# Kernel optimization log

Measured on AMD Instinct MI355X. Metric: run time of the kernel, lower is better.

The kernel has to match this reference:

```python
import jax, jax.numpy as jnp
import numpy as np

B, N, E = 256, 50000, 128000


def setup_inputs() -> dict:
    key = jax.random.key(0)
    ks = jax.random.split(key, 12)
    # forward args (normalized predictions / demand truth)
    pred_p_norm = jax.random.normal(ks[0], (B, N), dtype=jnp.float32)
    pred_f_norm = jax.random.normal(ks[1], (B, E), dtype=jnp.float32)
    true_d_norm = jax.random.normal(ks[2], (B, N), dtype=jnp.float32)
    # scaler params (positive scales)
    p_mean = jax.random.normal(ks[3], (N,), dtype=jnp.float32) * 10.0 + 50.0
    p_scale = jax.random.uniform(ks[4], (N,), dtype=jnp.float32, minval=0.5, maxval=5.0)
    f_mean = jax.random.normal(ks[5], (E,), dtype=jnp.float32) * 0.1
    f_scale = jax.random.uniform(ks[6], (E,), dtype=jnp.float32, minval=0.01, maxval=1.0)
    d_mean = jax.random.normal(ks[7], (N,), dtype=jnp.float32) * 0.01
    d_scale = jax.random.uniform(ks[8], (N,), dtype=jnp.float32, minval=0.001, maxval=0.1)
    node_elevation = jax.random.uniform(ks[9], (N,), dtype=jnp.float32, minval=0.0, maxval=300.0)
    # edge static attrs -> Hazen-Williams resistance R = 10.67 * L * (C+eps)^-1.852 * (D+eps)^-4.87
    L = jax.random.uniform(ks[10], (E,), dtype=jnp.float32, minval=10.0, maxval=1000.0)
    D = jax.random.uniform(ks[11], (E,), dtype=jnp.float32, minval=0.05, maxval=1.0)
    C = jnp.full((E,), 130.0, dtype=jnp.float32)
    eps = 1e-06
    R = 10.67 * L * (C + eps) ** (-1.852) * (D + eps) ** (-4.87)
    edge_index = jax.random.randint(jax.random.fold_in(key, 99), (2, E), 0, N, dtype=jnp.int32)
    return {
        'pred_p_norm': pred_p_norm, 'pred_f_norm': pred_f_norm, 'true_d_norm': true_d_norm,
        'p_mean': p_mean, 'p_scale': p_scale, 'f_mean': f_mean, 'f_scale': f_scale,
        'd_mean': d_mean, 'd_scale': d_scale, 'node_elevation': node_elevation,
        'R': R, 'edge_index': edge_index,
    }


def reference(pred_p_norm, pred_f_norm, true_d_norm, p_mean, p_scale, f_mean, f_scale,
              d_mean, d_scale, node_elevation, R, edge_index):
    n_nodes = pred_p_norm.shape[1]
    # denormalize (broadcast per-node / per-edge scalers over batch)
    P = pred_p_norm * p_scale[None, :] + p_mean[None, :]          # [B, N]
    Q = pred_f_norm * f_scale[None, :] + f_mean[None, :]          # [B, E]
    d = true_d_norm * d_scale[None, :] + d_mean[None, :]          # [B, N]
    H = P + node_elevation[None, :]                               # hydraulic head [B, N]
    src, dst = edge_index[0], edge_index[1]
    # mass conservation: net inflow per node vs demand
    Q_T = Q.T                                                      # [E, B]
    q_out = jax.ops.segment_sum(Q_T, src, num_segments=n_nodes).T  # [B, N]
    q_in = jax.ops.segment_sum(Q_T, dst, num_segments=n_nodes).T   # [B, N]
    q_net = q_in - q_out
    loss_mass = jnp.mean((q_net - d) ** 2)
    # head loss (Hazen-Williams): delta_h vs R*Q*|Q|^0.852
    h_src = H[:, src]                                              # [B, E]
    h_dst = H[:, dst]                                              # [B, E]
    delta_h_pred = h_src - h_dst
    friction_slope = R[None, :] * Q * jnp.abs(Q) ** 0.852
    loss_head = jnp.mean((delta_h_pred - friction_slope) ** 2)
    return (loss_mass, loss_head)
```

## Files before the change

kernel.cpp:

```cpp
#include <hip/hip_runtime.h>
#include <hip/hip_fp16.h>

#define TILE 64

__global__ void k_build_ht(const float* __restrict__ pred_p,
                           const float* __restrict__ p_scale,
                           const float* __restrict__ p_mean,
                           const float* __restrict__ elev,
                           const float* __restrict__ true_d,
                           const float* __restrict__ d_scale,
                           const float* __restrict__ d_mean,
                           __half* __restrict__ HTh,
                           __half* __restrict__ TD,
                           int B, int N) {
    __shared__ __align__(16) float tile[TILE][TILE + 2];
    const int n0 = blockIdx.x * TILE;
    const int b0 = blockIdx.y * TILE;
    const int tn = threadIdx.x % TILE;
    const int tw = threadIdx.x / TILE;
    const int c  = threadIdx.x & 31;
    const int rg = threadIdx.x >> 5;
    const int n = n0 + tn;

    {
        float sc = 0.f, mn = 0.f, el = 0.f;
        if (n < N) { sc = p_scale[n]; mn = p_mean[n]; el = elev[n]; }
        #pragma unroll
        for (int i = 0; i < TILE / 4; ++i) {
            const int bl = i * 4 + tw;
            float v = 0.f;
            if (n < N) v = pred_p[(size_t)(b0 + bl) * N + n] * sc + mn + el;
            tile[tn][bl] = v;
        }
        __syncthreads();
        #pragma unroll
        for (int i = 0; i < 8; ++i) {
            const int nl = i * 8 + rg;
            const int nn = n0 + nl;
            if (nn < N) {
                const float2 f = *reinterpret_cast<const float2*>(&tile[nl][2 * c]);
                reinterpret_cast<__half2*>(HTh + (size_t)nn * B + b0)[c] =
                    __floats2half2_rn(f.x, f.y);
            }
        }
    }
    __syncthreads();
    {
        float sc = 0.f, mn = 0.f;
        if (n < N) { sc = d_scale[n]; mn = d_mean[n]; }
        #pragma unroll
        for (int i = 0; i < TILE / 4; ++i) {
            const int bl = i * 4 + tw;
            float v = 0.f;
            if (n < N) v = true_d[(size_t)(b0 + bl) * N + n] * sc + mn;
            tile[tn][bl] = v;
        }
        __syncthreads();
        #pragma unroll
        for (int i = 0; i < 8; ++i) {
            const int nl = i * 8 + rg;
            const int nn = n0 + nl;
            if (nn < N) {
                const float2 f = *reinterpret_cast<const float2*>(&tile[nl][2 * c]);
                reinterpret_cast<__half2*>(TD + (size_t)nn * B + b0)[c] =
                    __floats2half2_rn(f.x, f.y);
            }
        }
    }
}

__global__ void k_hist(const int* __restrict__ nodes, int* __restrict__ deg, int M) {
    const int i = blockIdx.x * 256 + threadIdx.x;
    if (i < M) atomicAdd(&deg[nodes[i]], 1);
}

__global__ void k_scan1(const int* __restrict__ deg, int* __restrict__ bsum, int N) {
    __shared__ int s[256];
    const int i = blockIdx.x * 256 + threadIdx.x;
    s[threadIdx.x] = (i < N) ? deg[i] : 0;
    __syncthreads();
    #pragma unroll
    for (int off = 128; off >= 1; off >>= 1) {
        if (threadIdx.x < off) s[threadIdx.x] += s[threadIdx.x + off];
        __syncthreads();
    }
    if (threadIdx.x == 0) bsum[blockIdx.x] = s[0];
}

__global__ void k_scan2(int* __restrict__ bsum, int nb) {
    __shared__ int s[256];
    const int t = threadIdx.x;
    const int v = (t < nb) ? bsum[t] : 0;
    s[t] = v;
    __syncthreads();
    #pragma unroll
    for (int off = 1; off < 256; off <<= 1) {
        const int tmp = (t >= off) ? s[t - off] : 0;
        __syncthreads();
        s[t] += tmp;
        __syncthreads();
    }
    if (t < nb) bsum[t] = s[t] - v;
}

__global__ void k_scan3(const int* __restrict__ deg, const int* __restrict__ bsum,
                        int* __restrict__ offsets, int* __restrict__ cursor, int N) {
    __shared__ int s[256];
    const int t = threadIdx.x;
    const int i = blockIdx.x * 256 + t;
    const int v = (i < N) ? deg[i] : 0;
    s[t] = v;
    __syncthreads();
    #pragma unroll
    for (int off = 1; off < 256; off <<= 1) {
        const int tmp = (t >= off) ? s[t - off] : 0;
        __syncthreads();
        s[t] += tmp;
        __syncthreads();
    }
    const int excl = s[t] - v + bsum[blockIdx.x];
    if (i < N) { offsets[i] = excl; cursor[i] = excl; }
    if (i == N - 1) offsets[N] = excl + v;
}

__global__ void k_fill(const int* __restrict__ esrc, const int* __restrict__ edst,
                       int* __restrict__ cursor, int* __restrict__ inc, int E) {
    const int e = blockIdx.x * 256 + threadIdx.x;
    if (e < E) {
        const int ps = atomicAdd(&cursor[esrc[e]], 1);
        inc[ps] = (e << 1);
        const int pd = atomicAdd(&cursor[edst[e]], 1);
        inc[pd] = (e << 1) | 1;
    }
}

__global__ void k_edges(const float* __restrict__ pred_f,
                        const float* __restrict__ f_scale,
                        const float* __restrict__ f_mean,
                        const float* __restrict__ Rcoef,
                        const int* __restrict__ esrc,
                        const int* __restrict__ edst,
                        const __half* __restrict__ HTh,
                        __half* __restrict__ QT,
                        double* __restrict__ headp,
                        int B, int E) {
    __shared__ __align__(16) float qt[TILE][TILE + 2];
    __shared__ double wsum[4];
    const int e0 = blockIdx.x * TILE;
    const int b0 = blockIdx.y * TILE;
    const int te = threadIdx.x % TILE;
    const int tw = threadIdx.x / TILE;

    const int e = e0 + te;
    const float fs = f_scale[e];
    const float fm = f_mean[e];
    #pragma unroll
    for (int i = 0; i < TILE / 4; ++i) {
        const int bl = i * 4 + tw;
        qt[te][bl] = pred_f[(size_t)(b0 + bl) * E + e] * fs + fm;
    }
    __syncthreads();

    const int bl = te;
    const __half* HTb = HTh + b0 + bl;

    int   sarr[16], darr[16];
    float hs[16], hd[16];
    #pragma unroll
    for (int j = 0; j < 16; ++j) {
        const int ee = e0 + tw * 16 + j;
        sarr[j] = esrc[ee];
        darr[j] = edst[ee];
        hs[j] = __half2float(HTb[(size_t)sarr[j] * B]);
        hd[j] = __half2float(HTb[(size_t)darr[j] * B]);
    }

    const int sel = bl >> 5;
    const int pc  = bl & 31;
    #pragma unroll
    for (int k = 0; k < 8; ++k) {
        const int el = tw * 16 + 2 * k + sel;
        const float2 q01 = *reinterpret_cast<const float2*>(&qt[el][2 * pc]);
        const __half2 h = __floats2half2_rn(q01.x, q01.y);
        *reinterpret_cast<__half2*>(
            (char*)QT + (size_t)(e0 + el) * B * 2 + (size_t)b0 * 2 + pc * 4) = h;
    }

    double head = 0.0;
    #pragma unroll
    for (int j = 0; j < 16; ++j) {
        const int el = tw * 16 + j;
        const int ee = e0 + el;
        const float q = qt[el][bl];
        const float aq = fabsf(q);
        const float pw = exp2f(0.852f * __log2f(aq));
        const float fr = Rcoef[ee] * q * pw;
        const float t = (hs[j] - hd[j]) - fr;
        head += (double)t * (double)t;
    }

    #pragma unroll
    for (int off = 32; off >= 1; off >>= 1)
        head += __shfl_down(head, off, 64);
    if ((threadIdx.x & 63) == 0) wsum[threadIdx.x >> 6] = head;
    __syncthreads();
    if (threadIdx.x == 0)
        headp[(size_t)blockIdx.y * gridDim.x + blockIdx.x] =
            wsum[0] + wsum[1] + wsum[2] + wsum[3];
}

__global__ __launch_bounds__(256) void k_nodemass(
        const __half* __restrict__ QT,
        const __half* __restrict__ TD,
        const int* __restrict__ offsets,
        const int* __restrict__ inc,
        double* __restrict__ massp,
        int N) {
    __shared__ double wsum[4];
    const int w = threadIdx.x >> 6;
    const int lane = threadIdx.x & 63;
    const int n = blockIdx.x * 4 + w;

    double m = 0.0;
    if (n < N) {
        const uint2 tdr = *reinterpret_cast<const uint2*>(
            (const char*)TD + (size_t)n * 512 + (size_t)lane * 8);

        const int beg = offsets[n];
        const int end = offsets[n + 1];

        float qn0 = 0.f, qn1 = 0.f, qn2 = 0.f, qn3 = 0.f;
        for (int k = beg; k < end; k += 8) {
            int   ivv[8];
            float sg[8];
            uint2 vv[8];
            #pragma unroll
            for (int u = 0; u < 8; ++u) {
                const int kk = (k + u < end) ? (k + u) : (end - 1);
                ivv[u] = inc[kk];
                sg[u] = (k + u < end) ? ((ivv[u] & 1) ? 1.f : -1.f) : 0.f;
                vv[u] = *reinterpret_cast<const uint2*>(
                    (const char*)QT + (size_t)(ivv[u] >> 1) * 512
                                    + (size_t)lane * 8);
            }
            #pragma unroll
            for (int u = 0; u < 8; ++u) {
                const __half2 a = *reinterpret_cast<const __half2*>(&vv[u].x);
                const __half2 b = *reinterpret_cast<const __half2*>(&vv[u].y);
                const float2 fa = __half22float2(a);
                const float2 fb = __half22float2(b);
                qn0 += sg[u] * fa.x; qn1 += sg[u] * fa.y;
                qn2 += sg[u] * fb.x; qn3 += sg[u] * fb.y;
            }
        }

        const __half2 d01 = *reinterpret_cast<const __half2*>(&tdr.x);
        const __half2 d23 = *reinterpret_cast<const __half2*>(&tdr.y);
        const float2 f01 = __half22float2(d01);
        const float2 f23 = __half22float2(d23);
        const float t0 = qn0 - f01.x;
        const float t1 = qn1 - f01.y;
        const float t2 = qn2 - f23.x;
        const float t3 = qn3 - f23.y;
        m = (double)t0 * t0 + (double)t1 * t1
          + (double)t2 * t2 + (double)t3 * t3;
    }

    #pragma unroll
    for (int off = 32; off >= 1; off >>= 1)
        m += __shfl_down(m, off, 64);
    if (lane == 0) wsum[w] = m;
    __syncthreads();
    if (threadIdx.x == 0)
        massp[blockIdx.x] = wsum[0] + wsum[1] + wsum[2] + wsum[3];
}

__global__ void k_reduce(const double* __restrict__ massp, int nm,
                         const double* __restrict__ headp, int nh,
                         float* __restrict__ out,
                         double inv_mass, double inv_head) {
    __shared__ double sh[256];
    const int t = threadIdx.x;

    double s = 0.0;
    for (int i = t; i < nm; i += 256) s += massp[i];
    sh[t] = s;
    __syncthreads();
    #pragma unroll
    for (int off = 128; off >= 1; off >>= 1) {
        if (t < off) sh[t] += sh[t + off];
        __syncthreads();
    }
    double mass_total = 0.0;
    if (t == 0) mass_total = sh[0];
    __syncthreads();

    s = 0.0;
    for (int i = t; i < nh; i += 256) s += headp[i];
    sh[t] = s;
    __syncthreads();
    #pragma unroll
    for (int off = 128; off >= 1; off >>= 1) {
        if (t < off) sh[t] += sh[t + off];
        __syncthreads();
    }
    if (t == 0) {
        out[0] = (float)(mass_total * inv_mass);
        out[1] = (float)(sh[0] * inv_head);
    }
}

static inline size_t align256s(size_t x) { return (x + 255) & ~(size_t)255; }

extern "C" void kernel_launch(void* const* d_in, const int* in_sizes, int n_in,
                              void* d_out, int out_size, void* d_ws, size_t ws_size,
                              hipStream_t stream) {
    const float* pred_p  = (const float*)d_in[0];
    const float* pred_f  = (const float*)d_in[1];
    const float* true_d  = (const float*)d_in[2];
    const float* p_mean  = (const float*)d_in[3];
    const float* p_scale = (const float*)d_in[4];
    const float* f_mean  = (const float*)d_in[5];
    const float* f_scale = (const float*)d_in[6];
    const float* d_mean  = (const float*)d_in[7];
    const float* d_scale = (const float*)d_in[8];
    const float* elev    = (const float*)d_in[9];
    const float* Rcoef   = (const float*)d_in[10];
    const int*   eidx    = (const int*)d_in[11];

    const int N = in_sizes[3];
    const int E = in_sizes[10];
    const int B = in_sizes[0] / N;

    const int* esrc = eidx;
    const int* edst = eidx + E;

    const int gn = (N + TILE - 1) / TILE;
    const int gb = B / TILE;
    const int ge = E / TILE;
    const int nbk = (N + 255) / 256;
    const int nmB = (N + 3) / 4;

    char* ws = (char*)d_ws;
    size_t off = 0;
    __half* HTh   = (__half*)(ws + off); off = align256s(off + (size_t)N * B * 2);
    __half* TD    = (__half*)(ws + off); off = align256s(off + (size_t)N * B * 2);
    __half* QT    = (__half*)(ws + off); off = align256s(off + (size_t)E * B * 2);
    int* incarr   = (int*)(ws + off);    off = align256s(off + (size_t)2 * E * 4);
    int* offsets  = (int*)(ws + off);    off = align256s(off + (size_t)(N + 1) * 4);
    int* cursor   = (int*)(ws + off);    off = align256s(off + (size_t)N * 4);
    double* headp = (double*)(ws + off); off = align256s(off + (size_t)ge * gb * 8);
    double* massp = (double*)(ws + off); off = align256s(off + (size_t)nmB * 8);
    const size_t zero_beg = off;
    int* deg      = (int*)(ws + off);    off = align256s(off + (size_t)N * 4);
    int* bsum     = (int*)(ws + off);    off = align256s(off + 256 * 4);
    const size_t zero_len = off - zero_beg;

    hipMemsetAsync(ws + zero_beg, 0, zero_len, stream);

    k_hist <<<(2 * E + 255) / 256, 256, 0, stream>>>(eidx, deg, 2 * E);
    k_scan1<<<nbk, 256, 0, stream>>>(deg, bsum, N);
    k_scan2<<<1, 256, 0, stream>>>(bsum, nbk);
    k_scan3<<<nbk, 256, 0, stream>>>(deg, bsum, offsets, cursor, N);
    k_fill <<<(E + 255) / 256, 256, 0, stream>>>(esrc, edst, cursor, incarr, E);

    k_build_ht<<<dim3(gn, gb), 256, 0, stream>>>(pred_p, p_scale, p_mean, elev,
                                                 true_d, d_scale, d_mean,
                                                 HTh, TD, B, N);
    k_edges<<<dim3(ge, gb), 256, 0, stream>>>(pred_f, f_scale, f_mean, Rcoef,
                                              esrc, edst, HTh, QT,
                                              headp, B, E);
    k_nodemass<<<nmB, 256, 0, stream>>>(QT, TD, offsets, incarr, massp, N);
    k_reduce<<<1, 256, 0, stream>>>(massp, nmB, headp, ge * gb,
                                    (float*)d_out,
                                    1.0 / ((double)B * (double)N),
                                    1.0 / ((double)B * (double)E));
}
```

Measured before the change: 181.0 us.

## Restructure edge kernel over full batch, fuse histogram into build kernel

The edge kernel now processes all 256 batch columns per block. It stages Q as half in shared memory and gathers 8-byte rows of H per lane, so each src/dst index is read once instead of being re-gathered for each of four batch tiles with scalar half loads. The degree histogram is folded into the H/TD build kernel to remove one launch, and the node-mass kernel gets a short path for nodes with four or fewer incident edges. The cost is larger shared memory per block (about 50 KB) and fewer blocks in the edge kernel, which may lower occupancy.

```diff
diff --git a/kernel.cpp b/kernel.cpp
--- a/kernel.cpp
+++ b/kernel.cpp
@@ -10,6 +10,9 @@
                            const float* __restrict__ true_d,
                            const float* __restrict__ d_scale,
                            const float* __restrict__ d_mean,
+                           const int* __restrict__ nodes,
+                           int* __restrict__ deg,
+                           int M,
                            __half* __restrict__ HTh,
                            __half* __restrict__ TD,
                            int B, int N) {
@@ -22,6 +25,12 @@
     const int rg = threadIdx.x >> 5;
     const int n = n0 + tn;
 
+    const int flat = blockIdx.y * gridDim.x + blockIdx.x;
+    if (flat < (M + 255) / 256) {
+        const int i = flat * 256 + threadIdx.x;
+        if (i < M) atomicAdd(&deg[nodes[i]], 1);
+    }
+
     {
         float sc = 0.f, mn = 0.f, el = 0.f;
         if (n < N) { sc = p_scale[n]; mn = p_mean[n]; el = elev[n]; }
@@ -69,11 +78,6 @@
     }
 }
 
-__global__ void k_hist(const int* __restrict__ nodes, int* __restrict__ deg, int M) {
-    const int i = blockIdx.x * 256 + threadIdx.x;
-    if (i < M) atomicAdd(&deg[nodes[i]], 1);
-}
-
 __global__ void k_scan1(const int* __restrict__ deg, int* __restrict__ bsum, int N) {
     __shared__ int s[256];
     const int i = blockIdx.x * 256 + threadIdx.x;
@@ -134,69 +138,95 @@
     }
 }
 
-__global__ void k_edges(const float* __restrict__ pred_f,
-                        const float* __restrict__ f_scale,
-                        const float* __restrict__ f_mean,
-                        const float* __restrict__ Rcoef,
-                        const int* __restrict__ esrc,
-                        const int* __restrict__ edst,
-                        const __half* __restrict__ HTh,
-                        __half* __restrict__ QT,
-                        double* __restrict__ headp,
-                        int B, int E) {
-    __shared__ __align__(16) float qt[TILE][TILE + 2];
+__global__ __launch_bounds__(256) void k_edges(
+        const float* __restrict__ pred_f,
+        const float* __restrict__ f_scale,
+        const float* __restrict__ f_mean,
+        const float* __restrict__ Rcoef,
+        const int* __restrict__ esrc,
+        const int* __restrict__ edst,
+        const __half* __restrict__ HTh,
+        __half* __restrict__ QT,
+        double* __restrict__ headp,
+        int E) {
+    __shared__ __align__(16) float tile[TILE][TILE + 2];
+    __shared__ __align__(16) __half qth[TILE][268];
     __shared__ double wsum[4];
     const int e0 = blockIdx.x * TILE;
-    const int b0 = blockIdx.y * TILE;
-    const int te = threadIdx.x % TILE;
-    const int tw = threadIdx.x / TILE;
-
-    const int e = e0 + te;
+    const int tn = threadIdx.x & 63;
+    const int tw = threadIdx.x >> 6;
+    const int c  = threadIdx.x & 31;
+    const int rg = threadIdx.x >> 5;
+
+    const int e = e0 + tn;
     const float fs = f_scale[e];
     const float fm = f_mean[e];
-    #pragma unroll
-    for (int i = 0; i < TILE / 4; ++i) {
-        const int bl = i * 4 + tw;
-        qt[te][bl] = pred_f[(size_t)(b0 + bl) * E + e] * fs + fm;
-    }
-    __syncthreads();
-
-    const int bl = te;
-    const __half* HTb = HTh + b0 + bl;
-
-    int   sarr[16], darr[16];
-    float hs[16], hd[16];
-    #pragma unroll
-    for (int j = 0; j < 16; ++j) {
-        const int ee = e0 + tw * 16 + j;
-        sarr[j] = esrc[ee];
-        darr[j] = edst[ee];
-        hs[j] = __half2float(HTb[(size_t)sarr[j] * B]);
-        hd[j] = __half2float(HTb[(size_t)darr[j] * B]);
-    }
-
-    const int sel = bl >> 5;
-    const int pc  = bl & 31;
-    #pragma unroll
-    for (int k = 0; k < 8; ++k) {
-        const int el = tw * 16 + 2 * k + sel;
-        const float2 q01 = *reinterpret_cast<const float2*>(&qt[el][2 * pc]);
-        const __half2 h = __floats2half2_rn(q01.x, q01.y);
-        *reinterpret_cast<__half2*>(
-            (char*)QT + (size_t)(e0 + el) * B * 2 + (size_t)b0 * 2 + pc * 4) = h;
-    }
-
-    double head = 0.0;
+
+    for (int sb = 0; sb < 4; ++sb) {
+        #pragma unroll
+        for (int i = 0; i < 16; ++i) {
+            const int bl = i * 4 + tw;
+            tile[tn][bl] = pred_f[(size_t)(sb * 64 + bl) * E + e] * fs + fm;
+        }
+        __syncthreads();
+        #pragma unroll
+        for (int i = 0; i < 8; ++i) {
+            const int el = i * 8 + rg;
+            const float2 f2 = *reinterpret_cast<const float2*>(&tile[el][2 * c]);
+            *reinterpret_cast<__half2*>(&qth[el][sb * 64 + 2 * c]) =
+                __floats2half2_rn(f2.x, f2.y);
+        }
+        __syncthreads();
+    }
+
+    uint2 hsv[16], hdv[16];
+    float Rv[16];
     #pragma unroll
     for (int j = 0; j < 16; ++j) {
         const int el = tw * 16 + j;
         const int ee = e0 + el;
-        const float q = qt[el][bl];
-        const float aq = fabsf(q);
-        const float pw = exp2f(0.852f * __log2f(aq));
-        const float fr = Rcoef[ee] * q * pw;
-        const float t = (hs[j] - hd[j]) - fr;
-        head += (double)t * (double)t;
+        const int s = esrc[ee];
+        const int d = edst[ee];
+        Rv[j] = Rcoef[ee];
+        hsv[j] = *reinterpret_cast<const uint2*>(
+            (const char*)HTh + (size_t)s * 512 + (size_t)tn * 8);
+        hdv[j] = *reinterpret_cast<const uint2*>(
+            (const char*)HTh + (size_t)d * 512 + (size_t)tn * 8);
+        const uint2 q4 = *reinterpret_cast<const uint2*>(
+            (const char*)&qth[el][0] + (size_t)tn * 8);
+        *reinterpret_cast<uint2*>(
+            (char*)QT + (size_t)ee * 512 + (size_t)tn * 8) = q4;
+    }
+
+    double head = 0.0;
+    #pragma unroll
+    for (int j = 0; j < 16; ++j) {
+        const int el = tw * 16 + j;
+        const uint2 q4 = *reinterpret_cast<const uint2*>(
+            (const char*)&qth[el][0] + (size_t)tn * 8);
+        const __half2 qa = *reinterpret_cast<const __half2*>(&q4.x);
+        const __half2 qb = *reinterpret_cast<const __half2*>(&q4.y);
+        const __half2 sa = *reinterpret_cast<const __half2*>(&hsv[j].x);
+        const __half2 sb2 = *reinterpret_cast<const __half2*>(&hsv[j].y);
+        const __half2 da = *reinterpret_cast<const __half2*>(&hdv[j].x);
+        const __half2 db = *reinterpret_cast<const __half2*>(&hdv[j].y);
+        const float2 qf0 = __half22float2(qa), qf1 = __half22float2(qb);
+        const float2 sf0 = __half22float2(sa), sf1 = __half22float2(sb2);
+        const float2 df0 = __half22float2(da), df1 = __half22float2(db);
+        const float R = Rv[j];
+
+        float qv[4] = {qf0.x, qf0.y, qf1.x, qf1.y};
+        float sv[4] = {sf0.x, sf0.y, sf1.x, sf1.y};
+        float dv[4] = {df0.x, df0.y, df1.x, df1.y};
+        #pragma unroll
+        for (int r = 0; r < 4; ++r) {
+            const float q = qv[r];
+            const float aq = fabsf(q);
+            const float pw = exp2f(0.852f * __log2f(aq));
+            const float fr = R * q * pw;
+            const float t = (sv[r] - dv[r]) - fr;
+            head += (double)t * (double)t;
+        }
     }
 
     #pragma unroll
@@ -205,8 +235,7 @@
     if ((threadIdx.x & 63) == 0) wsum[threadIdx.x >> 6] = head;
     __syncthreads();
     if (threadIdx.x == 0)
-        headp[(size_t)blockIdx.y * gridDim.x + blockIdx.x] =
-            wsum[0] + wsum[1] + wsum[2] + wsum[3];
+        headp[blockIdx.x] = wsum[0] + wsum[1] + wsum[2] + wsum[3];
 }
 
 __global__ __launch_bounds__(256) void k_nodemass(
@@ -228,29 +257,54 @@
 
         const int beg = offsets[n];
         const int end = offsets[n + 1];
+        const int cnt = end - beg;
 
         float qn0 = 0.f, qn1 = 0.f, qn2 = 0.f, qn3 = 0.f;
-        for (int k = beg; k < end; k += 8) {
-            int   ivv[8];
-            float sg[8];
-            uint2 vv[8];
+        if (cnt <= 4) {
+            int   ivv[4];
+            float sg[4];
+            uint2 vv[4];
             #pragma unroll
-            for (int u = 0; u < 8; ++u) {
-                const int kk = (k + u < end) ? (k + u) : (end - 1);
+            for (int u = 0; u < 4; ++u) {
+                const int kk = (beg + u < end) ? (beg + u) : (end - 1);
                 ivv[u] = inc[kk];
-                sg[u] = (k + u < end) ? ((ivv[u] & 1) ? 1.f : -1.f) : 0.f;
+                sg[u] = (beg + u < end) ? ((ivv[u] & 1) ? 1.f : -1.f) : 0.f;
                 vv[u] = *reinterpret_cast<const uint2*>(
                     (const char*)QT + (size_t)(ivv[u] >> 1) * 512
                                     + (size_t)lane * 8);
             }
             #pragma unroll
-            for (int u = 0; u < 8; ++u) {
+            for (int u = 0; u < 4; ++u) {
                 const __half2 a = *reinterpret_cast<const __half2*>(&vv[u].x);
                 const __half2 b = *reinterpret_cast<const __half2*>(&vv[u].y);
                 const float2 fa = __half22float2(a);
                 const float2 fb = __half22float2(b);
                 qn0 += sg[u] * fa.x; qn1 += sg[u] * fa.y;
                 qn2 += sg[u] * fb.x; qn3 += sg[u] * fb.y;
+            }
+        } else {
+            for (int k = beg; k < end; k += 8) {
+                int   ivv[8];
+                float sg[8];
+                uint2 vv[8];
+                #pragma unroll
+                for (int u = 0; u < 8; ++u) {
+                    const int kk = (k + u < end) ? (k + u) : (end - 1);
+                    ivv[u] = inc[kk];
+                    sg[u] = (k + u < end) ? ((ivv[u] & 1) ? 1.f : -1.f) : 0.f;
+                    vv[u] = *reinterpret_cast<const uint2*>(
+                        (const char*)QT + (size_t)(ivv[u] >> 1) * 512
+                                        + (size_t)lane * 8);
+                }
+                #pragma unroll
+                for (int u = 0; u < 8; ++u) {
+                    const __half2 a = *reinterpret_cast<const __half2*>(&vv[u].x);
+                    const __half2 b = *reinterpret_cast<const __half2*>(&vv[u].y);
+                    const float2 fa = __half22float2(a);
+                    const float2 fb = __half22float2(b);
+                    qn0 += sg[u] * fa.x; qn1 += sg[u] * fa.y;
+                    qn2 += sg[u] * fb.x; qn3 += sg[u] * fb.y;
+                }
             }
         }
 
@@ -349,7 +403,7 @@
     int* incarr   = (int*)(ws + off);    off = align256s(off + (size_t)2 * E * 4);
     int* offsets  = (int*)(ws + off);    off = align256s(off + (size_t)(N + 1) * 4);
     int* cursor   = (int*)(ws + off);    off = align256s(off + (size_t)N * 4);
-    double* headp = (double*)(ws + off); off = align256s(off + (size_t)ge * gb * 8);
+    double* headp = (double*)(ws + off); off = align256s(off + (size_t)ge * 8);
     double* massp = (double*)(ws + off); off = align256s(off + (size_t)nmB * 8);
     const size_t zero_beg = off;
     int* deg      = (int*)(ws + off);    off = align256s(off + (size_t)N * 4);
@@ -358,20 +412,19 @@
 
     hipMemsetAsync(ws + zero_beg, 0, zero_len, stream);
 
-    k_hist <<<(2 * E + 255) / 256, 256, 0, stream>>>(eidx, deg, 2 * E);
+    k_build_ht<<<dim3(gn, gb), 256, 0, stream>>>(pred_p, p_scale, p_mean, elev,
+                                                 true_d, d_scale, d_mean,
+                                                 eidx, deg, 2 * E,
+                                                 HTh, TD, B, N);
     k_scan1<<<nbk, 256, 0, stream>>>(deg, bsum, N);
     k_scan2<<<1, 256, 0, stream>>>(bsum, nbk);
     k_scan3<<<nbk, 256, 0, stream>>>(deg, bsum, offsets, cursor, N);
     k_fill <<<(E + 255) / 256, 256, 0, stream>>>(esrc, edst, cursor, incarr, E);
 
-    k_build_ht<<<dim3(gn, gb), 256, 0, stream>>>(pred_p, p_scale, p_mean, elev,
-                                                 true_d, d_scale, d_mean,
-                                                 HTh, TD, B, N);
-    k_edges<<<dim3(ge, gb), 256, 0, stream>>>(pred_f, f_scale, f_mean, Rcoef,
-                                              esrc, edst, HTh, QT,
-                                              headp, B, E);
+    k_edges<<<ge, 256, 0, stream>>>(pred_f, f_scale, f_mean, Rcoef,
+                                    esrc, edst, HTh, QT, headp, E);
     k_nodemass<<<nmB, 256, 0, stream>>>(QT, TD, offsets, incarr, massp, N);
-    k_reduce<<<1, 256, 0, stream>>>(massp, nmB, headp, ge * gb,
+    k_reduce<<<1, 256, 0, stream>>>(massp, nmB, headp, ge,
                                     (float*)d_out,
                                     1.0 / ((double)B * (double)N),
                                     1.0 / ((double)B * (double)E));
```

Result: faster. 176.2 us (-2.6%).
